# Kernel optimization log

Hardware: AMD Instinct MI355X
Metric: run time of the kernel (lower is better)

## Reference

```python
import jax, jax.numpy as jnp
import numpy as np

B, T, IMG, PS, D, DEPTH, NH = 1, 8, 224, 16, 768, 12, 12
HP = IMG // PS
NP = HP * HP          # 196 patches per frame
N = NP + 1            # +1 cls token per frame
DH = D // NH
MLP = 4 * D
SCALE = DH ** -0.5


def _ln(x, g, b):
    mu = x.mean(-1, keepdims=True)
    var = ((x - mu) ** 2).mean(-1, keepdims=True)
    return (x - mu) / jnp.sqrt(var + 1e-5) * g + b


def _forward(x, W_patch, b_patch, cls_token, pos_embed,
             ln1_g, ln1_b, qkv_w, qkv_b, proj_w, proj_b,
             ln2_g, ln2_b, fc1_w, fc1_b, fc2_w, fc2_b, lnf_g, lnf_b):
    Bc = x.shape[0]
    # --- patch embed (Conv3d k=(1,ps,ps), stride=(1,ps,ps) == per-frame patch matmul) ---
    p = x.reshape(Bc, T, 3, HP, PS, HP, PS).transpose(0, 1, 3, 5, 2, 4, 6)
    p = p.reshape(Bc, T, NP, 3 * PS * PS)
    emb = p @ W_patch.T + b_patch                     # [B,T,NP,D] (correct layout)
    # replicate torch flatten(3)/transpose(1,2)/reshape axis scramble:
    emb = jnp.swapaxes(emb, 2, 3).reshape(Bc, T, NP, D)
    cls = jnp.broadcast_to(cls_token.reshape(1, 1, 1, D), (Bc, T, 1, D))
    h = jnp.concatenate([cls, emb], axis=2) + pos_embed.reshape(1, 1, N, D)
    h = h.reshape(Bc, T * N, D)

    for i in range(DEPTH):
        # --- attention ---
        a = _ln(h, ln1_g[i], ln1_b[i])
        qkv = (a @ qkv_w[i] + qkv_b[i]).reshape(Bc, T * N, 3, NH, DH)
        q, k, v = (jnp.transpose(qkv[:, :, j], (0, 2, 1, 3)) for j in range(3))  # [B,H,S,dh]
        if i % 2 == 0:  # divided space-time
            qf = q.reshape(Bc, NH, T, N, DH)
            kf = k.reshape(Bc, NH, T, N, DH)
            vf = v.reshape(Bc, NH, T, N, DH)
            q_t = qf.mean(3, keepdims=True)           # [B,H,T,1,dh]
            k_t = kf.mean(3, keepdims=True)
            v_t = vf.mean(3, keepdims=True)
            attn_t = jax.nn.softmax(jnp.einsum('bhtqd,bhtkd->bhtqk', q_t, k_t) * SCALE, -1)
            x_t = jnp.einsum('bhtqk,bhtkd->bhtqd', attn_t, v_t)[:, :, :, 0]  # [B,H,T,dh]
            attn_s = jax.nn.softmax(jnp.einsum('bhtqd,bhtkd->bhtqk', qf, kf) * SCALE, -1)
            x_s = jnp.einsum('bhtqk,bhtkd->bhtqd', attn_s, vf)               # [B,H,T,N,dh]
            o = (x_s + x_t[:, :, :, None, :]).reshape(Bc, NH, T * N, DH)
        else:  # joint space-time
            attn = jax.nn.softmax(jnp.einsum('bhqd,bhkd->bhqk', q, k) * SCALE, -1)
            o = jnp.einsum('bhqk,bhkd->bhqd', attn, v)
        o = jnp.transpose(o, (0, 2, 1, 3)).reshape(Bc, T * N, D)
        h = h + (o @ proj_w[i] + proj_b[i])
        # --- mlp ---
        m = _ln(h, ln2_g[i], ln2_b[i])
        m = jax.nn.gelu(m @ fc1_w[i] + fc1_b[i], approximate=False)
        h = h + (m @ fc2_w[i] + fc2_b[i])

    return _ln(h, lnf_g, lnf_b).reshape(Bc, T, N, D)


def setup_inputs() -> dict:
    key = jax.random.key(0)
    ks = jax.random.split(key, 12)
    s = 0.02
    return {
        'x': jax.random.normal(ks[0], (B, T, 3, IMG, IMG), jnp.float32),
        'W_patch': jax.random.normal(ks[1], (D, 3 * PS * PS), jnp.float32) * s,
        'b_patch': jnp.zeros((D,), jnp.float32),
        'cls_token': jax.random.normal(ks[2], (1, 1, D), jnp.float32) * s,
        'pos_embed': jax.random.normal(ks[3], (1, N, D), jnp.float32) * s,
        'ln1_g': jnp.ones((DEPTH, D), jnp.float32),
        'ln1_b': jnp.zeros((DEPTH, D), jnp.float32),
        'qkv_w': jax.random.normal(ks[4], (DEPTH, D, 3 * D), jnp.float32) * s,
        'qkv_b': jnp.zeros((DEPTH, 3 * D), jnp.float32),
        'proj_w': jax.random.normal(ks[5], (DEPTH, D, D), jnp.float32) * s,
        'proj_b': jnp.zeros((DEPTH, D), jnp.float32),
        'ln2_g': jnp.ones((DEPTH, D), jnp.float32),
        'ln2_b': jnp.zeros((DEPTH, D), jnp.float32),
        'fc1_w': jax.random.normal(ks[6], (DEPTH, D, MLP), jnp.float32) * s,
        'fc1_b': jnp.zeros((DEPTH, MLP), jnp.float32),
        'fc2_w': jax.random.normal(ks[7], (DEPTH, MLP, D), jnp.float32) * s,
        'fc2_b': jnp.zeros((DEPTH, D), jnp.float32),
        'lnf_g': jnp.ones((D,), jnp.float32),
        'lnf_b': jnp.zeros((D,), jnp.float32),
    }


def reference(x, W_patch, b_patch, cls_token, pos_embed,
              ln1_g, ln1_b, qkv_w, qkv_b, proj_w, proj_b,
              ln2_g, ln2_b, fc1_w, fc1_b, fc2_w, fc2_b, lnf_g, lnf_b):
    return _forward(x, W_patch, b_patch, cls_token, pos_embed,
                    ln1_g, ln1_b, qkv_w, qkv_b, proj_w, proj_b,
                    ln2_g, ln2_b, fc1_w, fc1_b, fc2_w, fc2_b, lnf_g, lnf_b)
```

## Files before the change

kernel.cpp:

```cpp
#include <hip/hip_runtime.h>
#include <math.h>

#define Dm 768
#define Tn 8
#define Nn 197
#define Sn 1576
#define MLPn 3072
#define NPn 196
#define MPAD 1664

typedef unsigned short u16;
typedef __bf16 bf16x8 __attribute__((ext_vector_type(8)));
typedef float f32x4 __attribute__((ext_vector_type(4)));
typedef unsigned int u32x4 __attribute__((ext_vector_type(4)));
typedef u16 u16x8 __attribute__((ext_vector_type(8)));
typedef u16 u16x4 __attribute__((ext_vector_type(4)));

__device__ inline u16 f2bf(float f) {
    union { float f; unsigned u; } v; v.f = f;
    unsigned r = v.u + 0x7fffu + ((v.u >> 16) & 1u);
    return (u16)(r >> 16);
}
__device__ inline float bf2f(u16 v) {
    union { unsigned u; float f; } x; x.u = ((unsigned)v) << 16; return x.f;
}

__device__ __forceinline__ void gl_lds16(const u16* __restrict__ g, u16* l) {
    __builtin_amdgcn_global_load_lds((const __attribute__((address_space(1))) void*)g,
                                     (__attribute__((address_space(3))) void*)l,
                                     16, 0, 0);
}

__global__ __launch_bounds__(256) void im2col_k(const float* __restrict__ x, u16* __restrict__ P) {
    int idx = blockIdx.x * 256 + threadIdx.x;
    if (idx >= 1568 * 768) return;
    int c = idx % 768, r = idx / 768;
    int p = r % 196, t = r / 196;
    int hp = p / 14, wp = p % 14;
    int ch = c / 256, rem = c % 256, py = rem / 16, px = rem % 16;
    P[idx] = f2bf(x[((t * 3 + ch) * 224 + hp * 16 + py) * 224 + wp * 16 + px]);
}

__global__ __launch_bounds__(256) void cvt_k(const float* __restrict__ s, u16* __restrict__ d, int n) {
    int i = blockIdx.x * 256 + threadIdx.x;
    if (i < n) d[i] = f2bf(s[i]);
}

__global__ __launch_bounds__(256) void cvtT_layer_k(const float* __restrict__ qw, const float* __restrict__ pw,
                                                    const float* __restrict__ f1w, const float* __restrict__ f2w,
                                                    u16* __restrict__ Wq, u16* __restrict__ Wp,
                                                    u16* __restrict__ W1, u16* __restrict__ W2) {
    __shared__ float tile[32][33];
    int bid = blockIdx.x;
    const float* src; u16* dst; int K, N, k0, n0;
    if (bid < 1728)      { src = qw;  dst = Wq; K = 768;  N = 2304; int r = bid;        k0 = (r / 72) * 32; n0 = (r % 72) * 32; }
    else if (bid < 2304) { src = pw;  dst = Wp; K = 768;  N = 768;  int r = bid - 1728; k0 = (r / 24) * 32; n0 = (r % 24) * 32; }
    else if (bid < 4608) { src = f1w; dst = W1; K = 768;  N = 3072; int r = bid - 2304; k0 = (r / 96) * 32; n0 = (r % 96) * 32; }
    else                 { src = f2w; dst = W2; K = 3072; N = 768;  int r = bid - 4608; k0 = (r / 24) * 32; n0 = (r % 24) * 32; }
    int tx = threadIdx.x & 31, ty = threadIdx.x >> 5;
#pragma unroll
    for (int i = 0; i < 4; ++i) tile[ty + 8 * i][tx] = src[(size_t)(k0 + ty + 8 * i) * N + n0 + tx];
    __syncthreads();
#pragma unroll
    for (int i = 0; i < 4; ++i) dst[(size_t)(n0 + ty + 8 * i) * K + k0 + tx] = f2bf(tile[tx][ty + 8 * i]);
}

__global__ __launch_bounds__(256) void build_h_k(const float* __restrict__ emb, const float* __restrict__ cls,
                                                 const float* __restrict__ pos, float* __restrict__ h) {
    int idx = blockIdx.x * 256 + threadIdx.x;
    if (idx >= Sn * Dm) return;
    int d = idx % Dm, s = idx / Dm;
    int t = s / Nn, r = s % Nn;
    float v;
    if (r == 0) v = cls[d];
    else {
        int f = (r - 1) * Dm + d;
        int p = f % NPn, dd = f / NPn;
        v = emb[(size_t)(t * NPn + p) * Dm + dd];
    }
    h[idx] = v + pos[r * Dm + d];
}

template <typename OutT>
__global__ __launch_bounds__(256) void ln_k(const float* __restrict__ X, const float* __restrict__ g,
                                            const float* __restrict__ bta, OutT* __restrict__ Y) {
    int row = blockIdx.x;
    const float* x = X + (size_t)row * Dm;
    float s = 0.f, s2 = 0.f;
#pragma unroll
    for (int q = 0; q < 3; ++q) {
        float v = x[threadIdx.x + q * 256];
        s += v; s2 += v * v;
    }
#pragma unroll
    for (int off = 1; off < 64; off <<= 1) {
        s  += __shfl_xor(s,  off);
        s2 += __shfl_xor(s2, off);
    }
    __shared__ float red[8];
    int wv = threadIdx.x >> 6;
    if ((threadIdx.x & 63) == 0) { red[wv * 2] = s; red[wv * 2 + 1] = s2; }
    __syncthreads();
    s  = red[0] + red[2] + red[4] + red[6];
    s2 = red[1] + red[3] + red[5] + red[7];
    float mu  = s * (1.f / 768.f);
    float var = s2 * (1.f / 768.f) - mu * mu;
    float rstd = rsqrtf(var + 1e-5f);
#pragma unroll
    for (int q = 0; q < 3; ++q) {
        int i = threadIdx.x + q * 256;
        float v = (x[i] - mu) * rstd * g[i] + bta[i];
        if constexpr (sizeof(OutT) == 2) Y[(size_t)row * Dm + i] = f2bf(v);
        else                             Y[(size_t)row * Dm + i] = v;
    }
}

__global__ __launch_bounds__(256) void mgemm_k(const u16* __restrict__ A, const u16* __restrict__ Bt,
                                               float* __restrict__ Cp, int N, int Kfull, int Kc) {
    __shared__ __align__(16) u16 As[4096];
    __shared__ __align__(16) u16 Bs[4096];
    int split = blockIdx.z;
    A  += split * Kc;
    Bt += split * Kc;
    Cp += (size_t)split * MPAD * N;
    int tid = threadIdx.x;
    int lane = tid & 63, w = tid >> 6;
    int wm = w & 1, wn = w >> 1;
    int m0 = blockIdx.y * 128, n0 = blockIdx.x * 128;
    f32x4 acc[4][4] = {};
    int c0 = tid, c1 = tid + 256;
    int ar0 = ((c0 >> 6) << 4) + (c0 & 15), ac0 = ((c0 >> 4) & 3) << 3;
    int ar1 = ((c1 >> 6) << 4) + (c1 & 15), ac1 = ((c1 >> 4) & 3) << 3;
    const u16* Arow0 = A  + (size_t)(m0 + ar0) * Kfull + ac0;
    const u16* Arow1 = A  + (size_t)(m0 + ar1) * Kfull + ac1;
    const u16* Brow0 = Bt + (size_t)(n0 + ar0) * Kfull + ac0;
    const u16* Brow1 = Bt + (size_t)(n0 + ar1) * Kfull + ac1;
    u16* As0 = As + (w * 64) * 8;
    u16* As1 = As + (256 + w * 64) * 8;
    u16* Bs0 = Bs + (w * 64) * 8;
    u16* Bs1 = Bs + (256 + w * 64) * 8;
    for (int k0 = 0; k0 < Kc; k0 += 32) {
        gl_lds16(Arow0 + k0, As0);
        gl_lds16(Arow1 + k0, As1);
        gl_lds16(Brow0 + k0, Bs0);
        gl_lds16(Brow1 + k0, Bs1);
        __syncthreads();
        bf16x8 af[4], bfr[4];
#pragma unroll
        for (int i = 0; i < 4; ++i) {
            af[i]  = *(const bf16x8*)(As + (((wm * 4 + i) * 64 + lane) << 3));
            bfr[i] = *(const bf16x8*)(Bs + (((wn * 4 + i) * 64 + lane) << 3));
        }
#pragma unroll
        for (int mi = 0; mi < 4; ++mi)
#pragma unroll
            for (int ni = 0; ni < 4; ++ni)
                acc[mi][ni] = __builtin_amdgcn_mfma_f32_16x16x32_bf16(af[mi], bfr[ni], acc[mi][ni], 0, 0, 0);
        __syncthreads();
    }
    int rbase = (lane >> 4) << 2, cl = lane & 15;
#pragma unroll
    for (int mi = 0; mi < 4; ++mi)
#pragma unroll
        for (int r = 0; r < 4; ++r) {
            int gm = m0 + wm * 64 + mi * 16 + rbase + r;
#pragma unroll
            for (int ni = 0; ni < 4; ++ni) {
                int gn = n0 + wn * 64 + ni * 16 + cl;
                Cp[(size_t)gm * N + gn] = acc[mi][ni][r];
            }
        }
}

template <bool GELU_ACT, bool RESID, typename OutT>
__global__ __launch_bounds__(256) void ep_k(const float* __restrict__ Cp, const float* __restrict__ bias,
                                            const float* __restrict__ resid, OutT* __restrict__ out,
                                            int N, int S) {
    int row = blockIdx.y;
    int n = blockIdx.x * 1024 + threadIdx.x * 4;
    if (n >= N) return;
    size_t off = (size_t)row * N + n;
    f32x4 acc = *(const f32x4*)(Cp + off);
    for (int s = 1; s < S; ++s)
        acc += *(const f32x4*)(Cp + (size_t)s * MPAD * N + off);
    acc += *(const f32x4*)(bias + n);
    if (GELU_ACT) {
#pragma unroll
        for (int j = 0; j < 4; ++j) acc[j] = 0.5f * acc[j] * (1.f + erff(acc[j] * 0.7071067811865476f));
    }
    if (RESID) acc += *(const f32x4*)(resid + off);
    if constexpr (sizeof(OutT) == 2) {
        u16x4 o;
#pragma unroll
        for (int j = 0; j < 4; ++j) o[j] = f2bf(acc[j]);
        *(u16x4*)((u16*)out + off) = o;
    } else {
        *(f32x4*)((float*)out + off) = acc;
    }
}

__global__ __launch_bounds__(64) void vmean_k(const u16* __restrict__ qkv, float* __restrict__ vm) {
    int g = blockIdx.x;
    int h = g >> 3, t = g & 7;
    int d = threadIdx.x;
    float s = 0.f;
    for (int n = 0; n < Nn; ++n)
        s += bf2f(qkv[(size_t)(t * Nn + n) * 2304 + 1536 + h * 64 + d]);
    vm[g * 64 + d] = s * (1.f / 197.f);
}

__global__ __launch_bounds__(256) void attn_mfma_k(const u16* __restrict__ qkv, float* __restrict__ Ou,
                                                   float* __restrict__ ml, int even, int nsplit,
                                                   int NG, int Sq) {
    __shared__ __align__(16) u16 Ks[64 * 64];
    __shared__ __align__(16) u16 Vt[64 * 64];
    __shared__ __align__(16) u16 Ps[4 * 32 * 64];
    int g = blockIdx.y;
    int h, sbase;
    if (even) { h = g >> 3; sbase = (g & 7) * Nn; } else { h = g; sbase = 0; }
    int split = blockIdx.z;
    int chunk = (Sq + nsplit - 1) / nsplit;
    int kbeg = split * chunk, kend = min(Sq, kbeg + chunk);
    int tid = threadIdx.x, lane = tid & 63, w = tid >> 6;
    int quad = lane >> 4, l15 = lane & 15;
    int q0w = blockIdx.x * 128 + w * 32;
    u16* Pw = Ps + w * 2048;

    bf16x8 aq[2][2];
#pragma unroll
    for (int mb = 0; mb < 2; ++mb) {
        int qidx = q0w + mb * 16 + l15; if (qidx >= Sq) qidx = Sq - 1;
        const u16* qp = qkv + (size_t)(sbase + qidx) * 2304 + h * 64;
#pragma unroll
        for (int ks = 0; ks < 2; ++ks)
            aq[mb][ks] = *(const bf16x8*)(qp + ks * 32 + quad * 8);
    }
    f32x4 acc_o[2][4] = {};
    float m_run[2][4], l_run[2][4];
#pragma unroll
    for (int mb = 0; mb < 2; ++mb)
#pragma unroll
        for (int r = 0; r < 4; ++r) { m_run[mb][r] = -INFINITY; l_run[mb][r] = 0.f; }

    for (int kt = kbeg; kt < kend; kt += 64) {
        int cnt = kend - kt; if (cnt > 64) cnt = 64;
        {
            int dc = tid & 7;
#pragma unroll
            for (int p = 0; p < 2; ++p) {
                int row = (tid >> 3) + 32 * p;
                u32x4 kd = {};
                if (row < cnt) kd = *(const u32x4*)(qkv + (size_t)(sbase + kt + row) * 2304 + 768 + h * 64 + dc * 8);
                *(u32x4*)(Ks + row * 64 + ((dc ^ (row & 7)) << 3)) = kd;
            }
        }
        {
            int d = (tid & 31) * 2, kc = tid >> 5;
            u16x8 lo, hi;
#pragma unroll
            for (int i = 0; i < 8; ++i) {
                int key = kc * 8 + i;
                unsigned t = 0;
                if (key < cnt) t = *(const unsigned*)(qkv + (size_t)(sbase + kt + key) * 2304 + 1536 + h * 64 + d);
                lo[i] = (u16)(t & 0xffffu); hi[i] = (u16)(t >> 16);
            }
            *(u16x8*)(Vt + d * 64 + ((kc ^ (d & 7)) << 3)) = lo;
            *(u16x8*)(Vt + (d + 1) * 64 + ((kc ^ ((d + 1) & 7)) << 3)) = hi;
        }
        __syncthreads();
        f32x4 acc_s[2][4] = {};
#pragma unroll
        for (int ni = 0; ni < 4; ++ni) {
            int key = l15 + ni * 16;
#pragma unroll
            for (int ks = 0; ks < 2; ++ks) {
                bf16x8 bk = *(const bf16x8*)(Ks + key * 64 + ((((ks << 2) + quad) ^ (key & 7)) << 3));
                acc_s[0][ni] = __builtin_amdgcn_mfma_f32_16x16x32_bf16(aq[0][ks], bk, acc_s[0][ni], 0, 0, 0);
                acc_s[1][ni] = __builtin_amdgcn_mfma_f32_16x16x32_bf16(aq[1][ks], bk, acc_s[1][ni], 0, 0, 0);
            }
        }
#pragma unroll
        for (int mb = 0; mb < 2; ++mb) {
#pragma unroll
            for (int ni = 0; ni < 4; ++ni) {
                int keyabs = kt + l15 + ni * 16;
#pragma unroll
                for (int r = 0; r < 4; ++r) {
                    float sv = acc_s[mb][ni][r] * 0.125f;
                    if (keyabs >= kend) sv = -1e30f;
                    acc_s[mb][ni][r] = sv;
                }
            }
#pragma unroll
            for (int r = 0; r < 4; ++r) {
                float mx = fmaxf(fmaxf(acc_s[mb][0][r], acc_s[mb][1][r]), fmaxf(acc_s[mb][2][r], acc_s[mb][3][r]));
                mx = fmaxf(mx, __shfl_xor(mx, 1));
                mx = fmaxf(mx, __shfl_xor(mx, 2));
                mx = fmaxf(mx, __shfl_xor(mx, 4));
                mx = fmaxf(mx, __shfl_xor(mx, 8));
                float mnew = fmaxf(m_run[mb][r], mx);
                float pv[4], ps = 0.f;
#pragma unroll
                for (int ni = 0; ni < 4; ++ni) { pv[ni] = __expf(acc_s[mb][ni][r] - mnew); ps += pv[ni]; }
                ps += __shfl_xor(ps, 1);
                ps += __shfl_xor(ps, 2);
                ps += __shfl_xor(ps, 4);
                ps += __shfl_xor(ps, 8);
                float alpha = __expf(m_run[mb][r] - mnew);
                l_run[mb][r] = l_run[mb][r] * alpha + ps;
                m_run[mb][r] = mnew;
#pragma unroll
                for (int ni = 0; ni < 4; ++ni) acc_o[mb][ni][r] *= alpha;
                int prow = mb * 16 + quad * 4 + r;
#pragma unroll
                for (int ni = 0; ni < 4; ++ni) {
                    int key = l15 + ni * 16;
                    Pw[prow * 64 + (((key >> 3) ^ (prow & 7)) << 3) + (key & 7)] = f2bf(pv[ni]);
                }
            }
        }
        bf16x8 ap[2][2];
#pragma unroll
        for (int mb = 0; mb < 2; ++mb)
#pragma unroll
            for (int ks = 0; ks < 2; ++ks)
                ap[mb][ks] = *(const bf16x8*)(Pw + (mb * 16 + l15) * 64 + ((((ks << 2) + quad) ^ (l15 & 7)) << 3));
#pragma unroll
        for (int ni = 0; ni < 4; ++ni) {
            int d = l15 + ni * 16;
#pragma unroll
            for (int ks = 0; ks < 2; ++ks) {
                bf16x8 bv = *(const bf16x8*)(Vt + d * 64 + ((((ks << 2) + quad) ^ (d & 7)) << 3));
                acc_o[0][ni] = __builtin_amdgcn_mfma_f32_16x16x32_bf16(ap[0][ks], bv, acc_o[0][ni], 0, 0, 0);
                acc_o[1][ni] = __builtin_amdgcn_mfma_f32_16x16x32_bf16(ap[1][ks], bv, acc_o[1][ni], 0, 0, 0);
            }
        }
        __syncthreads();
    }
    size_t gb = ((size_t)split * NG + g) * Sq;
#pragma unroll
    for (int mb = 0; mb < 2; ++mb)
#pragma unroll
        for (int r = 0; r < 4; ++r) {
            int q = q0w + mb * 16 + quad * 4 + r;
            if (q < Sq) {
                float* op = Ou + (gb + q) * 64;
#pragma unroll
                for (int ni = 0; ni < 4; ++ni) op[l15 + ni * 16] = acc_o[mb][ni][r];
                if (l15 == 0) {
                    ml[(gb + q) * 2]     = m_run[mb][r];
                    ml[(gb + q) * 2 + 1] = l_run[mb][r];
                }
            }
        }
}

__global__ __launch_bounds__(256) void comb_k(const float* __restrict__ Ou, const float* __restrict__ ml,
                                              const float* __restrict__ vm, u16* __restrict__ ob,
                                              int even, int nsplit, int NG, int Sq) {
    int g = blockIdx.y;
    int q = blockIdx.x * 4 + (threadIdx.x >> 6);
    int d = threadIdx.x & 63;
    if (q >= Sq) return;
    int h, sbase;
    if (even) { h = g >> 3; sbase = (g & 7) * Nn; } else { h = g; sbase = 0; }
    float M = -INFINITY;
    for (int s = 0; s < nsplit; ++s) M = fmaxf(M, ml[(((size_t)s * NG + g) * Sq + q) * 2]);
    float num = 0.f, den = 0.f;
    for (int s = 0; s < nsplit; ++s) {
        size_t base = ((size_t)s * NG + g) * Sq + q;
        float wgt = __expf(ml[base * 2] - M);
        den += wgt * ml[base * 2 + 1];
        num += wgt * Ou[base * 64 + d];
    }
    float o = num / den;
    if (even) o += vm[g * 64 + d];
    ob[(size_t)(sbase + q) * Dm + h * 64 + d] = f2bf(o);
}

extern "C" void kernel_launch(void* const* d_in, const int* in_sizes, int n_in,
                              void* d_out, int out_size, void* d_ws, size_t ws_size,
                              hipStream_t stream) {
    (void)in_sizes; (void)n_in; (void)out_size; (void)ws_size;
    const float* x       = (const float*)d_in[0];
    const float* W_patch = (const float*)d_in[1];
    const float* b_patch = (const float*)d_in[2];
    const float* cls     = (const float*)d_in[3];
    const float* pos     = (const float*)d_in[4];
    const float* ln1_g   = (const float*)d_in[5];
    const float* ln1_b   = (const float*)d_in[6];
    const float* qkv_w   = (const float*)d_in[7];
    const float* qkv_b   = (const float*)d_in[8];
    const float* proj_w  = (const float*)d_in[9];
    const float* proj_b  = (const float*)d_in[10];
    const float* ln2_g   = (const float*)d_in[11];
    const float* ln2_b   = (const float*)d_in[12];
    const float* fc1_w   = (const float*)d_in[13];
    const float* fc1_b   = (const float*)d_in[14];
    const float* fc2_w   = (const float*)d_in[15];
    const float* fc2_b   = (const float*)d_in[16];
    const float* lnf_g   = (const float*)d_in[17];
    const float* lnf_b   = (const float*)d_in[18];

    char* base = (char*)d_ws;
    auto alloc = [&](size_t bytes) { void* p = base; base += (bytes + 255) & ~(size_t)255; return p; };
    u16*   P    = (u16*)  alloc((size_t)MPAD * 768 * 2);
    u16*   Wq   = (u16*)  alloc((size_t)2304 * 768 * 2);
    u16*   Wp   = (u16*)  alloc((size_t)768 * 768 * 2);
    u16*   W1   = (u16*)  alloc((size_t)3072 * 768 * 2);
    u16*   W2   = (u16*)  alloc((size_t)768 * 3072 * 2);
    float* emb  = (float*)alloc((size_t)1568 * 768 * 4);
    float* h    = (float*)alloc((size_t)Sn * Dm * 4);
    u16*   a    = (u16*)  alloc((size_t)MPAD * 768 * 2);
    u16*   qkvb = (u16*)  alloc((size_t)Sn * 2304 * 2);
    u16*   ob   = (u16*)  alloc((size_t)MPAD * 768 * 2);
    u16*   mb   = (u16*)  alloc((size_t)MPAD * 3072 * 2);
    float* vm   = (float*)alloc((size_t)96 * 64 * 4);
    float* Ou   = (float*)alloc((size_t)3 * 12 * Sn * 64 * 4);
    float* ml   = (float*)alloc((size_t)3 * 12 * Sn * 2 * 4);
    float* Cp   = (float*)alloc((size_t)3 * MPAD * 2304 * 4);

    im2col_k<<<(1568 * 768 + 255) / 256, 256, 0, stream>>>(x, P);
    cvt_k<<<(768 * 768 + 255) / 256, 256, 0, stream>>>(W_patch, Wp, 768 * 768);
    mgemm_k<<<dim3(6, 13, 3), 256, 0, stream>>>(P, Wp, Cp, 768, 768, 256);
    ep_k<false, false, float><<<dim3(1, 1568), 256, 0, stream>>>(Cp, b_patch, nullptr, emb, 768, 3);
    build_h_k<<<(Sn * Dm + 255) / 256, 256, 0, stream>>>(emb, cls, pos, h);

    for (int i = 0; i < 12; ++i) {
        cvtT_layer_k<<<6912, 256, 0, stream>>>(
            qkv_w + (size_t)i * 768 * 2304, proj_w + (size_t)i * 768 * 768,
            fc1_w + (size_t)i * 768 * 3072, fc2_w + (size_t)i * 3072 * 768,
            Wq, Wp, W1, W2);
        ln_k<u16><<<Sn, 256, 0, stream>>>(h, ln1_g + i * Dm, ln1_b + i * Dm, a);
        mgemm_k<<<dim3(18, 13, 3), 256, 0, stream>>>(a, Wq, Cp, 2304, 768, 256);
        ep_k<false, false, u16><<<dim3(3, Sn), 256, 0, stream>>>(Cp, qkv_b + i * 2304, nullptr, qkvb, 2304, 3);
        if ((i & 1) == 0) {
            vmean_k<<<96, 64, 0, stream>>>(qkvb, vm);
            attn_mfma_k<<<dim3(2, 96, 1), 256, 0, stream>>>(qkvb, Ou, ml, 1, 1, 96, Nn);
            comb_k<<<dim3(50, 96), 256, 0, stream>>>(Ou, ml, vm, ob, 1, 1, 96, Nn);
        } else {
            attn_mfma_k<<<dim3(13, 12, 3), 256, 0, stream>>>(qkvb, Ou, ml, 0, 3, 12, Sn);
            comb_k<<<dim3(394, 12), 256, 0, stream>>>(Ou, ml, vm, ob, 0, 3, 12, Sn);
        }
        mgemm_k<<<dim3(6, 13, 4), 256, 0, stream>>>(ob, Wp, Cp, 768, 768, 192);
        ep_k<false, true, float><<<dim3(1, Sn), 256, 0, stream>>>(Cp, proj_b + i * Dm, h, h, 768, 4);
        ln_k<u16><<<Sn, 256, 0, stream>>>(h, ln2_g + i * Dm, ln2_b + i * Dm, a);
        mgemm_k<<<dim3(24, 13, 2), 256, 0, stream>>>(a, W1, Cp, 3072, 768, 384);
        ep_k<true, false, u16><<<dim3(3, Sn), 256, 0, stream>>>(Cp, fc1_b + i * MLPn, nullptr, mb, 3072, 2);
        mgemm_k<<<dim3(6, 13, 4), 256, 0, stream>>>(mb, W2, Cp, 768, 3072, 768);
        ep_k<false, true, float><<<dim3(1, Sn), 256, 0, stream>>>(Cp, fc2_b + i * Dm, h, h, 768, 4);
    }
    ln_k<float><<<Sn, 256, 0, stream>>>(h, lnf_g, lnf_b, (float*)d_out);
}
```

Measured before the change: 2.450 ms.

## Fuse bias/GELU epilogues into GEMMs and residual-add with LayerNorm

Adds a non-split-K 64x128 GEMM kernel that applies bias (and GELU for fc1) and writes bf16 directly, replacing the split-K GEMM plus separate epilogue for the QKV and fc1 projections. Merges the residual-add epilogue with the following LayerNorm into one row kernel, including the next layer's LN1 and the final LN. This removes the fp32 partial-sum round trips and several kernel launches per layer. The trade-off is that the fused GEMMs lose split-K parallelism, use a smaller tile, and have no double buffering.

```diff
diff --git a/kernel.cpp b/kernel.cpp
--- a/kernel.cpp
+++ b/kernel.cpp
@@ -172,10 +172,64 @@
         }
 }
 
-template <bool GELU_ACT, bool RESID, typename OutT>
+template <bool GELU_ACT>
+__global__ __launch_bounds__(256) void mgemm_fused_k(const u16* __restrict__ A, const u16* __restrict__ Bt,
+                                                     const float* __restrict__ bias, u16* __restrict__ out,
+                                                     int N, int Kfull, int Mout) {
+    __shared__ __align__(16) u16 As[64 * 32];
+    __shared__ __align__(16) u16 Bs[128 * 32];
+    int tid = threadIdx.x;
+    int lane = tid & 63, w = tid >> 6;
+    int wm = w & 1, wn = w >> 1;
+    int m0 = blockIdx.y * 64, n0 = blockIdx.x * 128;
+    f32x4 acc[2][4] = {};
+    int ca = tid;
+    int ar = ((ca >> 6) << 4) + (ca & 15), ac = ((ca >> 4) & 3) << 3;
+    const u16* Arow = A + (size_t)(m0 + ar) * Kfull + ac;
+    int cb1 = tid + 256;
+    int br1 = ((cb1 >> 6) << 4) + (cb1 & 15), bc1 = ((cb1 >> 4) & 3) << 3;
+    const u16* Brow0 = Bt + (size_t)(n0 + ar) * Kfull + ac;
+    const u16* Brow1 = Bt + (size_t)(n0 + br1) * Kfull + bc1;
+    u16* Asw  = As + (w * 64) * 8;
+    u16* Bsw0 = Bs + (w * 64) * 8;
+    u16* Bsw1 = Bs + (256 + w * 64) * 8;
+    for (int k0 = 0; k0 < Kfull; k0 += 32) {
+        gl_lds16(Arow + k0, Asw);
+        gl_lds16(Brow0 + k0, Bsw0);
+        gl_lds16(Brow1 + k0, Bsw1);
+        __syncthreads();
+        bf16x8 af[2], bfr[4];
+#pragma unroll
+        for (int i = 0; i < 2; ++i) af[i]  = *(const bf16x8*)(As + (((wm * 2 + i) * 64 + lane) << 3));
+#pragma unroll
+        for (int j = 0; j < 4; ++j) bfr[j] = *(const bf16x8*)(Bs + (((wn * 4 + j) * 64 + lane) << 3));
+#pragma unroll
+        for (int mi = 0; mi < 2; ++mi)
+#pragma unroll
+            for (int ni = 0; ni < 4; ++ni)
+                acc[mi][ni] = __builtin_amdgcn_mfma_f32_16x16x32_bf16(af[mi], bfr[ni], acc[mi][ni], 0, 0, 0);
+        __syncthreads();
+    }
+    int rbase = (lane >> 4) << 2, cl = lane & 15;
+#pragma unroll
+    for (int mi = 0; mi < 2; ++mi)
+#pragma unroll
+        for (int r = 0; r < 4; ++r) {
+            int gm = m0 + wm * 32 + mi * 16 + rbase + r;
+            if (gm < Mout) {
+#pragma unroll
+                for (int ni = 0; ni < 4; ++ni) {
+                    int gn = n0 + wn * 64 + ni * 16 + cl;
+                    float v = acc[mi][ni][r] + bias[gn];
+                    if (GELU_ACT) v = 0.5f * v * (1.f + erff(v * 0.7071067811865476f));
+                    out[(size_t)gm * N + gn] = f2bf(v);
+                }
+            }
+        }
+}
+
 __global__ __launch_bounds__(256) void ep_k(const float* __restrict__ Cp, const float* __restrict__ bias,
-                                            const float* __restrict__ resid, OutT* __restrict__ out,
-                                            int N, int S) {
+                                            float* __restrict__ out, int N, int S) {
     int row = blockIdx.y;
     int n = blockIdx.x * 1024 + threadIdx.x * 4;
     if (n >= N) return;
@@ -184,18 +238,47 @@
     for (int s = 1; s < S; ++s)
         acc += *(const f32x4*)(Cp + (size_t)s * MPAD * N + off);
     acc += *(const f32x4*)(bias + n);
-    if (GELU_ACT) {
-#pragma unroll
-        for (int j = 0; j < 4; ++j) acc[j] = 0.5f * acc[j] * (1.f + erff(acc[j] * 0.7071067811865476f));
-    }
-    if (RESID) acc += *(const f32x4*)(resid + off);
-    if constexpr (sizeof(OutT) == 2) {
-        u16x4 o;
-#pragma unroll
-        for (int j = 0; j < 4; ++j) o[j] = f2bf(acc[j]);
-        *(u16x4*)((u16*)out + off) = o;
-    } else {
-        *(f32x4*)((float*)out + off) = acc;
+    *(f32x4*)(out + off) = acc;
+}
+
+template <bool FINALOUT>
+__global__ __launch_bounds__(256) void ep_ln_k(const float* __restrict__ Cp, const float* __restrict__ bias,
+                                               float* __restrict__ h, const float* __restrict__ g,
+                                               const float* __restrict__ bta, void* __restrict__ lnout, int S) {
+    int row = blockIdx.x;
+    int t = threadIdx.x;
+    float v[3];
+    float s = 0.f, s2 = 0.f;
+#pragma unroll
+    for (int q = 0; q < 3; ++q) {
+        int i = t + q * 256;
+        size_t off = (size_t)row * Dm + i;
+        float a = Cp[off];
+        for (int sp = 1; sp < S; ++sp) a += Cp[(size_t)sp * MPAD * Dm + off];
+        a += bias[i] + h[off];
+        h[off] = a;
+        v[q] = a; s += a; s2 += a * a;
+    }
+#pragma unroll
+    for (int off = 1; off < 64; off <<= 1) {
+        s  += __shfl_xor(s,  off);
+        s2 += __shfl_xor(s2, off);
+    }
+    __shared__ float red[8];
+    int wv = t >> 6;
+    if ((t & 63) == 0) { red[wv * 2] = s; red[wv * 2 + 1] = s2; }
+    __syncthreads();
+    s  = red[0] + red[2] + red[4] + red[6];
+    s2 = red[1] + red[3] + red[5] + red[7];
+    float mu  = s * (1.f / 768.f);
+    float var = s2 * (1.f / 768.f) - mu * mu;
+    float rstd = rsqrtf(var + 1e-5f);
+#pragma unroll
+    for (int q = 0; q < 3; ++q) {
+        int i = t + q * 256;
+        float y = (v[q] - mu) * rstd * g[i] + bta[i];
+        if constexpr (FINALOUT) ((float*)lnout)[(size_t)row * Dm + i] = y;
+        else                    ((u16*)lnout)[(size_t)row * Dm + i] = f2bf(y);
     }
 }
 
@@ -418,22 +501,21 @@
     float* vm   = (float*)alloc((size_t)96 * 64 * 4);
     float* Ou   = (float*)alloc((size_t)3 * 12 * Sn * 64 * 4);
     float* ml   = (float*)alloc((size_t)3 * 12 * Sn * 2 * 4);
-    float* Cp   = (float*)alloc((size_t)3 * MPAD * 2304 * 4);
+    float* Cp   = (float*)alloc((size_t)4 * MPAD * 768 * 4);
 
     im2col_k<<<(1568 * 768 + 255) / 256, 256, 0, stream>>>(x, P);
     cvt_k<<<(768 * 768 + 255) / 256, 256, 0, stream>>>(W_patch, Wp, 768 * 768);
     mgemm_k<<<dim3(6, 13, 3), 256, 0, stream>>>(P, Wp, Cp, 768, 768, 256);
-    ep_k<false, false, float><<<dim3(1, 1568), 256, 0, stream>>>(Cp, b_patch, nullptr, emb, 768, 3);
+    ep_k<<<dim3(1, 1568), 256, 0, stream>>>(Cp, b_patch, emb, 768, 3);
     build_h_k<<<(Sn * Dm + 255) / 256, 256, 0, stream>>>(emb, cls, pos, h);
+    ln_k<u16><<<Sn, 256, 0, stream>>>(h, ln1_g, ln1_b, a);
 
     for (int i = 0; i < 12; ++i) {
         cvtT_layer_k<<<6912, 256, 0, stream>>>(
             qkv_w + (size_t)i * 768 * 2304, proj_w + (size_t)i * 768 * 768,
             fc1_w + (size_t)i * 768 * 3072, fc2_w + (size_t)i * 3072 * 768,
             Wq, Wp, W1, W2);
-        ln_k<u16><<<Sn, 256, 0, stream>>>(h, ln1_g + i * Dm, ln1_b + i * Dm, a);
-        mgemm_k<<<dim3(18, 13, 3), 256, 0, stream>>>(a, Wq, Cp, 2304, 768, 256);
-        ep_k<false, false, u16><<<dim3(3, Sn), 256, 0, stream>>>(Cp, qkv_b + i * 2304, nullptr, qkvb, 2304, 3);
+        mgemm_fused_k<false><<<dim3(18, 26), 256, 0, stream>>>(a, Wq, qkv_b + i * 2304, qkvb, 2304, 768, Sn);
         if ((i & 1) == 0) {
             vmean_k<<<96, 64, 0, stream>>>(qkvb, vm);
             attn_mfma_k<<<dim3(2, 96, 1), 256, 0, stream>>>(qkvb, Ou, ml, 1, 1, 96, Nn);
@@ -443,12 +525,12 @@
             comb_k<<<dim3(394, 12), 256, 0, stream>>>(Ou, ml, vm, ob, 0, 3, 12, Sn);
         }
         mgemm_k<<<dim3(6, 13, 4), 256, 0, stream>>>(ob, Wp, Cp, 768, 768, 192);
-        ep_k<false, true, float><<<dim3(1, Sn), 256, 0, stream>>>(Cp, proj_b + i * Dm, h, h, 768, 4);
-        ln_k<u16><<<Sn, 256, 0, stream>>>(h, ln2_g + i * Dm, ln2_b + i * Dm, a);
-        mgemm_k<<<dim3(24, 13, 2), 256, 0, stream>>>(a, W1, Cp, 3072, 768, 384);
-        ep_k<true, false, u16><<<dim3(3, Sn), 256, 0, stream>>>(Cp, fc1_b + i * MLPn, nullptr, mb, 3072, 2);
+        ep_ln_k<false><<<Sn, 256, 0, stream>>>(Cp, proj_b + i * Dm, h, ln2_g + i * Dm, ln2_b + i * Dm, a, 4);
+        mgemm_fused_k<true><<<dim3(24, 26), 256, 0, stream>>>(a, W1, fc1_b + i * MLPn, mb, 3072, 768, Sn);
         mgemm_k<<<dim3(6, 13, 4), 256, 0, stream>>>(mb, W2, Cp, 768, 3072, 768);
-        ep_k<false, true, float><<<dim3(1, Sn), 256, 0, stream>>>(Cp, fc2_b + i * Dm, h, h, 768, 4);
-    }
-    ln_k<float><<<Sn, 256, 0, stream>>>(h, lnf_g, lnf_b, (float*)d_out);
-}
+        if (i < 11)
+            ep_ln_k<false><<<Sn, 256, 0, stream>>>(Cp, fc2_b + i * Dm, h, ln1_g + (i + 1) * Dm, ln1_b + (i + 1) * Dm, a, 4);
+        else
+            ep_ln_k<true><<<Sn, 256, 0, stream>>>(Cp, fc2_b + i * Dm, h, lnf_g, lnf_b, d_out, 4);
+    }
+}
```

After: 2.369 ms. 3.3% less time.
